# Kernel optimization log

Measured on AMD Instinct MI355X. Metric: run time of the kernel, lower is better.

The kernel has to match this reference:

```python
import jax, jax.numpy as jnp
import numpy as np

D, H, DH = 768, 12, 64
W = 256            # one-sided window (attention_window=512 total)
EPS = 1e-6
NEG = -1e9


def layer_norm(x, g, b):
    m = jnp.mean(x, axis=-1, keepdims=True)
    v = jnp.mean((x - m) ** 2, axis=-1, keepdims=True)
    return g * (x - m) * jax.lax.rsqrt(v + EPS) + b


def _blocks3(t, nb):
    # t: [B,H,nb,W,dh] -> keys/values of 3 neighboring blocks [B,H,nb,3W,dh]
    tp = jnp.pad(t, ((0, 0), (0, 0), (1, 1), (0, 0), (0, 0)))
    return jnp.concatenate([tp[:, :, :nb], tp[:, :, 1:nb + 1], tp[:, :, 2:nb + 2]], axis=3)


def sliding_window_attention(x, kpm, Wq, bq, Wk, bk, Wv, bv, Wo, bo):
    B, S, _ = x.shape
    nb = S // W
    def proj(Wm, bm):
        return (x @ Wm + bm).reshape(B, S, H, DH).transpose(0, 2, 1, 3).reshape(B, H, nb, W, DH)
    q = proj(Wq, bq) * (1.0 / np.sqrt(DH))
    k = proj(Wk, bk)
    v = proj(Wv, bv)
    k3 = _blocks3(k, nb)
    v3 = _blocks3(v, nb)
    # scores over local band: [B,H,nb,W,3W]
    s = jnp.einsum('bhnqd,bhnkd->bhnqk', q, k3)
    qi = jnp.arange(W)[:, None]
    kj = jnp.arange(3 * W)[None, :]
    band = jnp.abs(kj - W - qi) <= W                     # [W,3W]
    kg = (jnp.arange(nb)[:, None, None] - 1) * W + kj[None]  # global key idx [nb,1,3W]
    inrange = (kg >= 0) & (kg < S)
    # key padding mask gathered into block layout: [B,nb,3W]
    kpm_b = jnp.pad(kpm.reshape(B, nb, W), ((0, 0), (1, 1), (0, 0)), constant_values=True)
    kpm3 = jnp.concatenate([kpm_b[:, :nb], kpm_b[:, 1:nb + 1], kpm_b[:, 2:nb + 2]], axis=2)
    m = band[None, None, None] & inrange[None, None] & (~kpm3)[:, None, :, None, :]
    s = jnp.where(m, s, NEG)
    p = jax.nn.softmax(s, axis=-1)
    o = jnp.einsum('bhnqk,bhnkd->bhnqd', p, v3)
    o = o.reshape(B, H, S, DH).transpose(0, 2, 1, 3).reshape(B, S, D)
    return o @ Wo + bo


def setup_inputs() -> dict:
    key = jax.random.key(0)
    ks = jax.random.split(key, 12)
    B, S, DF = 2, 4096, 3072
    sc = 1.0 / np.sqrt(D)
    return {
        'x': jax.random.normal(ks[0], (B, S, D), jnp.float32),
        'mask': jnp.zeros((B, S), bool),
        'id': 0,
        'Wq': jax.random.normal(ks[1], (D, D), jnp.float32) * sc,
        'bq': jnp.zeros((D,), jnp.float32),
        'Wk': jax.random.normal(ks[2], (D, D), jnp.float32) * sc,
        'bk': jnp.zeros((D,), jnp.float32),
        'Wv': jax.random.normal(ks[3], (D, D), jnp.float32) * sc,
        'bv': jnp.zeros((D,), jnp.float32),
        'Wo': jax.random.normal(ks[4], (D, D), jnp.float32) * sc,
        'bo': jnp.zeros((D,), jnp.float32),
        'ln1_g': jnp.ones((D,), jnp.float32),
        'ln1_b': jnp.zeros((D,), jnp.float32),
        'W1': jax.random.normal(ks[5], (D, DF), jnp.float32) * sc,
        'b1': jnp.zeros((DF,), jnp.float32),
        'W2': jax.random.normal(ks[6], (DF, D), jnp.float32) * (1.0 / np.sqrt(DF)),
        'b2': jnp.zeros((D,), jnp.float32),
        'ln2_g': jnp.ones((D,), jnp.float32),
        'ln2_b': jnp.zeros((D,), jnp.float32),
    }


def reference(x, mask, id, Wq, bq, Wk, bk, Wv, bv, Wo, bo, ln1_g, ln1_b, W1, b1, W2, b2, ln2_g, ln2_b):
    # Sublayer 1: pre-norm residual around sliding-window self-attention
    h = layer_norm(x, ln1_g, ln1_b)
    x = x + sliding_window_attention(h, mask, Wq, bq, Wk, bk, Wv, bv, Wo, bo)
    # Sublayer 2: pre-norm residual around positionwise FFN
    h = layer_norm(x, ln2_g, ln2_b)
    x = x + (jax.nn.relu(h @ W1 + b1) @ W2 + b2)
    return x
```

## Files before the change

kernel.cpp:

```cpp
#include <hip/hip_runtime.h>
#include <hip/hip_bf16.h>
#include <cstddef>

typedef __attribute__((ext_vector_type(8))) short short8;
typedef __attribute__((ext_vector_type(4))) float f32x4;
typedef __attribute__((ext_vector_type(4))) unsigned short us4;

typedef __attribute__((address_space(1))) void as1_void;
typedef __attribute__((address_space(3))) void as3_void;

__device__ __forceinline__ void gload16(const void* g, void* lds) {
  __builtin_amdgcn_global_load_lds((as1_void*)(void*)g, (as3_void*)lds, 16, 0, 0);
}

__device__ inline unsigned short f2bf(float f) {
  union { float f; unsigned int u; } v; v.f = f;
  return (unsigned short)((v.u + 0x7FFFu + ((v.u >> 16) & 1u)) >> 16);
}

__global__ __launch_bounds__(256) void ln_kernel(const float* __restrict__ x,
    const float* __restrict__ g, const float* __restrict__ b,
    unsigned short* __restrict__ out)
{
  int row = blockIdx.x, t = threadIdx.x;
  const float* xr = x + (size_t)row * 768;
  float v0 = xr[t], v1 = xr[t + 256], v2 = xr[t + 512];
  float s = v0 + v1 + v2;
  #pragma unroll
  for (int o = 32; o > 0; o >>= 1) s += __shfl_xor(s, o);
  __shared__ float r1[4], r2[4];
  if ((t & 63) == 0) r1[t >> 6] = s;
  __syncthreads();
  float mean = (r1[0] + r1[1] + r1[2] + r1[3]) * (1.0f / 768.0f);
  float d0 = v0 - mean, d1 = v1 - mean, d2 = v2 - mean;
  float q = d0 * d0 + d1 * d1 + d2 * d2;
  #pragma unroll
  for (int o = 32; o > 0; o >>= 1) q += __shfl_xor(q, o);
  if ((t & 63) == 0) r2[t >> 6] = q;
  __syncthreads();
  float var = (r2[0] + r2[1] + r2[2] + r2[3]) * (1.0f / 768.0f);
  float rs = rsqrtf(var + 1e-6f);
  unsigned short* orow = out + (size_t)row * 768;
  orow[t]       = f2bf(g[t]       * d0 * rs + b[t]);
  orow[t + 256] = f2bf(g[t + 256] * d1 * rs + b[t + 256]);
  orow[t + 512] = f2bf(g[t + 512] * d2 * rs + b[t + 512]);
}

__global__ __launch_bounds__(256) void transpose_kernel(const float* __restrict__ W,
    unsigned short* __restrict__ WT, int K, int N)
{
  __shared__ float tile[32][33];
  int tx = threadIdx.x & 31, ty = threadIdx.x >> 5;
  int k0 = blockIdx.x * 32, n0 = blockIdx.y * 32;
  #pragma unroll
  for (int i = 0; i < 32; i += 8)
    tile[ty + i][tx] = W[(size_t)(k0 + ty + i) * N + n0 + tx];
  __syncthreads();
  #pragma unroll
  for (int i = 0; i < 32; i += 8)
    WT[(size_t)(n0 + ty + i) * K + k0 + tx] = f2bf(tile[tx][ty + i]);
}

__global__ __launch_bounds__(256) void catbias_kernel(const float* __restrict__ bq,
    const float* __restrict__ bk, const float* __restrict__ bv, float* __restrict__ o)
{
  int i = blockIdx.x * 256 + threadIdx.x;
  o[i] = (i < 768) ? bq[i] : ((i < 1536) ? bk[i - 768] : bv[i - 1536]);
}

enum { EPI_QKV = 0, EPI_RELU = 1, EPI_RESID = 2 };

template<int EPI>
__global__ __launch_bounds__(512, 1) void gemmP_kernel(
    const unsigned short* __restrict__ A, const unsigned short* __restrict__ BT,
    const float* __restrict__ bias, const float* __restrict__ resid,
    void* __restrict__ outp, int M, int N, int K, int ntn)
{
  __shared__ char lds[2][49152];
  int tid = threadIdx.x;
  int nwg = gridDim.x;
  int bid = ((int)blockIdx.x & 7) * (nwg >> 3) + ((int)blockIdx.x >> 3);
  int mt = bid / ntn, nt = bid % ntn;
  int m0 = mt * 128, n0 = nt * 256;
  int w = tid >> 6, l = tid & 63;
  int wr = w >> 2, wc = w & 3;
  int fr = l & 15, fq = l >> 4;
  int swz = (fr >> 1) * 128 + (((((fr & 1) << 2) | fq) ^ ((fr >> 1) & 7)) << 4);
  int t8 = tid >> 3;
  int uu = (tid & 7) ^ (t8 & 7);
  int rb = 2 * t8 + (uu >> 2);
  int kb = (uu & 3) * 8;
  const unsigned short* Asrc  = A  + (size_t)(m0 + rb) * K + kb;
  const unsigned short* Bsrc0 = BT + (size_t)(n0 + rb) * K + kb;
  const unsigned short* Bsrc1 = BT + (size_t)(n0 + 128 + rb) * K + kb;

  auto stage = [&](int buf, int kt, int h) {
    int ko = kt * 64 + h * 32;
    char* dA = &lds[buf][0] + h * 8192 + (w << 10);
    char* dB = &lds[buf][16384] + h * 16384 + (w << 10);
    gload16(Asrc + ko, dA);
    gload16(Bsrc0 + ko, dB);
    gload16(Bsrc1 + ko, dB + 8192);
  };

  f32x4 acc[4][4] = {};

#define GP_COMPUTE(RBUF, H)                                                    \
  { short8 af[4], bf[4];                                                       \
    const char* ab_ = &lds[RBUF][0] + (H) * 8192 + wr * 4096 + swz;            \
    const char* bb_ = &lds[RBUF][16384] + (H) * 16384 + wc * 4096 + swz;       \
    _Pragma("unroll")                                                          \
    for (int i_ = 0; i_ < 4; i_++) af[i_] = *(const short8*)(ab_ + i_ * 1024); \
    _Pragma("unroll")                                                          \
    for (int j_ = 0; j_ < 4; j_++) bf[j_] = *(const short8*)(bb_ + j_ * 1024); \
    __builtin_amdgcn_s_setprio(1);                                             \
    _Pragma("unroll")                                                          \
    for (int i_ = 0; i_ < 4; i_++)                                             \
      _Pragma("unroll")                                                        \
      for (int j_ = 0; j_ < 4; j_++)                                           \
        acc[i_][j_] = __builtin_amdgcn_mfma_f32_16x16x32_bf16(                 \
            af[i_], bf[j_], acc[i_][j_], 0, 0, 0);                             \
    __builtin_amdgcn_s_setprio(0); }

  stage(0, 0, 0); stage(0, 0, 1);
  asm volatile("s_waitcnt vmcnt(3)" ::: "memory");
  __builtin_amdgcn_s_barrier();

  int NT = K >> 6;
  for (int t = 0; t < NT - 1; ++t) {
    int R = t & 1, W = R ^ 1;
    GP_COMPUTE(R, 0);
    stage(W, t + 1, 0);
    asm volatile("s_waitcnt vmcnt(3)" ::: "memory");
    __builtin_amdgcn_s_barrier();
    GP_COMPUTE(R, 1);
    stage(W, t + 1, 1);
    asm volatile("s_waitcnt vmcnt(3)" ::: "memory");
    __builtin_amdgcn_s_barrier();
  }
  {
    int R = (NT - 1) & 1;
    GP_COMPUTE(R, 0);
    asm volatile("s_waitcnt vmcnt(0)" ::: "memory");
    __builtin_amdgcn_s_barrier();
    GP_COMPUTE(R, 1);
  }
#undef GP_COMPUTE

  #pragma unroll
  for (int nj = 0; nj < 4; nj++) {
    int col = n0 + wc * 64 + nj * 16 + fr;
    float bs = bias[col];
    if (EPI == EPI_QKV) {
      int which = (col >= 1536) ? 2 : ((col >= 768) ? 1 : 0);
      int c2 = col - which * 768;
      int hh = c2 >> 6, dh = c2 & 63;
      if (which == 2) {
        unsigned short* dstv = reinterpret_cast<unsigned short*>(outp) + (size_t)2 * 8192 * 768;
        #pragma unroll
        for (int i = 0; i < 4; i++) {
          int row0 = m0 + wr * 64 + i * 16 + fq * 4;
          int bb = row0 >> 12, sl = row0 & 4095;
          us4 pv;
          #pragma unroll
          for (int r = 0; r < 4; r++) pv[r] = f2bf(acc[i][nj][r] + bs);
          *reinterpret_cast<us4*>(&dstv[((size_t)(bb * 12 + hh) * 64 + dh) * 4096 + sl]) = pv;
        }
      } else {
        unsigned short* dst = reinterpret_cast<unsigned short*>(outp) + (size_t)which * 8192 * 768;
        #pragma unroll
        for (int i = 0; i < 4; i++) {
          #pragma unroll
          for (int r = 0; r < 4; r++) {
            int row = m0 + wr * 64 + i * 16 + fq * 4 + r;
            float c = acc[i][nj][r] + bs;
            if (which == 0) c *= 0.125f;
            int bb = row >> 12, sl = row & 4095;
            dst[(((size_t)(bb * 12 + hh)) * 4096 + sl) * 64 + dh] = f2bf(c);
          }
        }
      }
    } else if (EPI == EPI_RELU) {
      #pragma unroll
      for (int i = 0; i < 4; i++)
        #pragma unroll
        for (int r = 0; r < 4; r++) {
          int row = m0 + wr * 64 + i * 16 + fq * 4 + r;
          float c = fmaxf(acc[i][nj][r] + bs, 0.0f);
          reinterpret_cast<unsigned short*>(outp)[(size_t)row * N + col] = f2bf(c);
        }
    } else {
      #pragma unroll
      for (int i = 0; i < 4; i++)
        #pragma unroll
        for (int r = 0; r < 4; r++) {
          int row = m0 + wr * 64 + i * 16 + fq * 4 + r;
          float c = acc[i][nj][r] + bs + resid[(size_t)row * N + col];
          reinterpret_cast<float*>(outp)[(size_t)row * N + col] = c;
        }
    }
  }
}

__global__ __launch_bounds__(256) void attn_fused_kernel(
    const unsigned short* __restrict__ qg, const unsigned short* __restrict__ kg,
    const unsigned short* __restrict__ vtg, const unsigned char* __restrict__ kpm,
    unsigned short* __restrict__ attn_out)
{
  __shared__ unsigned short lds_k[2][64 * 64];
  __shared__ unsigned short lds_vt[2][64 * 64];
  __shared__ unsigned short lds_p[4][32 * 64];
  int bid0 = blockIdx.x;
  int bid = (bid0 & 7) * 96 + (bid0 >> 3);
  int qblk = bid & 31, h = (bid >> 5) % 12, b = bid / 384;
  int bh = b * 12 + h;
  int q0 = qblk * 128;
  int tid = threadIdx.x, w = tid >> 6, l = tid & 63;
  int fr = l & 15, fq = l >> 4;
  int qw0 = q0 + w * 32;
  int swzb = (((l & 7) ^ (l >> 3)) << 4);
  const char* qbase  = (const char*)(qg  + (size_t)bh * 4096 * 64);
  const char* kbase  = (const char*)(kg  + (size_t)bh * 4096 * 64);
  const char* vtbase = (const char*)(vtg + (size_t)bh * 64 * 4096);
  const unsigned char* kpmb = kpm + (size_t)b * 4096;

  #pragma unroll
  for (int s = 0; s < 4; s++) {
    int row = w * 32 + s * 8 + (l >> 3);
    gload16(qbase + (size_t)(q0 + row) * 128 + swzb, (char*)lds_p[w] + s * 1024);
  }

  auto stageKV = [&](int c, int buf) {
    int g0 = q0 - 256 + c * 64;
    if (g0 < 0 || g0 >= 4096) return;
    #pragma unroll
    for (int s = 0; s < 2; s++) {
      int row = w * 16 + s * 8 + (l >> 3);
      gload16(kbase + (size_t)(g0 + row) * 128 + swzb,
              (char*)lds_k[buf] + (w * 2 + s) * 1024);
      gload16(vtbase + ((size_t)row * 4096 + g0) * 2 + swzb,
              (char*)lds_vt[buf] + (w * 2 + s) * 1024);
    }
  };

  stageKV(0, 0);
  asm volatile("s_waitcnt vmcnt(0)");
  __syncthreads();

  short8 qf[2][2];
  #pragma unroll
  for (int i = 0; i < 2; i++)
    #pragma unroll
    for (int ks = 0; ks < 2; ks++)
      qf[i][ks] = *(const short8*)((const char*)lds_p[w] + (i * 16 + fr) * 128 +
                    ((ks * 64 + fq * 16) ^ ((fr & 7) << 4)));

  f32x4 acc_o[2][4] = {};
  float m_st[2] = {-3.0e38f, -3.0e38f};
  float l_st[2] = {0.0f, 0.0f};

  for (int c = 0; c < 10; c++) {
    int g0 = q0 - 256 + c * 64;
    bool valid = (g0 >= 0) && (g0 < 4096);
    if (c < 9) stageKV(c + 1, (c + 1) & 1);
    if (valid) {
      int buf = c & 1;
      unsigned int km[4];
      #pragma unroll
      for (int j = 0; j < 4; j++)
        km[j] = *(const unsigned int*)(kpmb + g0 + 16 * j + 4 * fq);
      bool anyk = __any((km[0] | km[1] | km[2] | km[3]) != 0);
      int rel = g0 - qw0;
      bool edge = anyk || (rel < -225) || (rel > 193);
      short8 kf[4][2];
      #pragma unroll
      for (int j = 0; j < 4; j++)
        #pragma unroll
        for (int ks = 0; ks < 2; ks++)
          kf[j][ks] = *(const short8*)((const char*)lds_k[buf] + (j * 16 + fr) * 128 +
                        ((ks * 64 + fq * 16) ^ ((fr & 7) << 4)));
      f32x4 accs[4][2] = {};
      #pragma unroll
      for (int j = 0; j < 4; j++)
        #pragma unroll
        for (int i = 0; i < 2; i++)
          #pragma unroll
          for (int ks = 0; ks < 2; ks++)
            accs[j][i] = __builtin_amdgcn_mfma_f32_16x16x32_bf16(kf[j][ks], qf[i][ks], accs[j][i], 0, 0, 0);
      #pragma unroll
      for (int i = 0; i < 2; i++) {
        float sv[4][4];
        #pragma unroll
        for (int j = 0; j < 4; j++)
          #pragma unroll
          for (int r = 0; r < 4; r++)
            sv[j][r] = accs[j][i][r];
        if (edge) {
          int base = rel + 4 * fq - fr - 16 * i;
          #pragma unroll
          for (int j = 0; j < 4; j++)
            #pragma unroll
            for (int r = 0; r < 4; r++) {
              int d = base + 16 * j + r;
              bool ok = (d >= -256) && (d <= 256) && (((km[j] >> (8 * r)) & 255u) == 0u);
              if (!ok) sv[j][r] = -1.0e9f;
            }
        }
        float mv = sv[0][0];
        #pragma unroll
        for (int j = 0; j < 4; j++)
          #pragma unroll
          for (int r = 0; r < 4; r++) mv = fmaxf(mv, sv[j][r]);
        mv = fmaxf(mv, __shfl_xor(mv, 16));
        mv = fmaxf(mv, __shfl_xor(mv, 32));
        float mo = m_st[i];
        float mn = fmaxf(mo, mv);
        float scl = __expf(mo - mn);
        float rs = 0.0f;
        unsigned int pk[4][2];
        #pragma unroll
        for (int j = 0; j < 4; j++) {
          float p0 = __expf(sv[j][0] - mn), p1 = __expf(sv[j][1] - mn);
          float p2 = __expf(sv[j][2] - mn), p3 = __expf(sv[j][3] - mn);
          rs += (p0 + p1) + (p2 + p3);
          pk[j][0] = (unsigned)f2bf(p0) | ((unsigned)f2bf(p1) << 16);
          pk[j][1] = (unsigned)f2bf(p2) | ((unsigned)f2bf(p3) << 16);
        }
        rs += __shfl_xor(rs, 16);
        rs += __shfl_xor(rs, 32);
        l_st[i] = l_st[i] * scl + rs;
        m_st[i] = mn;
        char* prow = (char*)lds_p[w] + (i * 16 + fr) * 128;
        #pragma unroll
        for (int j = 0; j < 4; j++) {
          uint2 u; u.x = pk[j][0]; u.y = pk[j][1];
          *(uint2*)(prow + ((32 * j + 8 * fq) ^ ((fr & 7) << 4))) = u;
        }
        #pragma unroll
        for (int r = 0; r < 4; r++) {
          float so = __shfl(scl, (l & 48) | ((l >> 2) & 12) | r);
          #pragma unroll
          for (int jd = 0; jd < 4; jd++) acc_o[i][jd][r] *= so;
        }
      }
      short8 pf[2][2];
      #pragma unroll
      for (int i = 0; i < 2; i++)
        #pragma unroll
        for (int ks = 0; ks < 2; ks++)
          pf[i][ks] = *(const short8*)((const char*)lds_p[w] + (i * 16 + fr) * 128 +
                        ((ks * 64 + fq * 16) ^ ((fr & 7) << 4)));
      short8 vf[4][2];
      #pragma unroll
      for (int jd = 0; jd < 4; jd++)
        #pragma unroll
        for (int ks = 0; ks < 2; ks++)
          vf[jd][ks] = *(const short8*)((const char*)lds_vt[buf] + (jd * 16 + fr) * 128 +
                        ((ks * 64 + fq * 16) ^ ((fr & 7) << 4)));
      #pragma unroll
      for (int i = 0; i < 2; i++)
        #pragma unroll
        for (int jd = 0; jd < 4; jd++)
          #pragma unroll
          for (int ks = 0; ks < 2; ks++)
            acc_o[i][jd] = __builtin_amdgcn_mfma_f32_16x16x32_bf16(pf[i][ks], vf[jd][ks], acc_o[i][jd], 0, 0, 0);
    }
    asm volatile("s_waitcnt vmcnt(0)");
    __syncthreads();
  }
  #pragma unroll
  for (int i = 0; i < 2; i++) {
    #pragma unroll
    for (int r = 0; r < 4; r++) {
      float lv = __shfl(l_st[i], (l & 48) | ((l >> 2) & 12) | r);
      float inv = 1.0f / lv;
      int qrow = qw0 + i * 16 + fq * 4 + r;
      size_t orow = ((size_t)b * 4096 + qrow) * 768 + h * 64;
      #pragma unroll
      for (int jd = 0; jd < 4; jd++)
        attn_out[orow + jd * 16 + fr] = f2bf(acc_o[i][jd][r] * inv);
    }
  }
}

extern "C" void kernel_launch(void* const* d_in, const int* in_sizes, int n_in,
                              void* d_out, int out_size, void* d_ws, size_t ws_size,
                              hipStream_t stream) {
  const float* x            = (const float*)d_in[0];
  const unsigned char* mask = (const unsigned char*)d_in[1];
  const float* Wq  = (const float*)d_in[3];
  const float* bq  = (const float*)d_in[4];
  const float* Wk  = (const float*)d_in[5];
  const float* bk  = (const float*)d_in[6];
  const float* Wv  = (const float*)d_in[7];
  const float* bv  = (const float*)d_in[8];
  const float* Wo  = (const float*)d_in[9];
  const float* bo  = (const float*)d_in[10];
  const float* ln1g = (const float*)d_in[11];
  const float* ln1b = (const float*)d_in[12];
  const float* W1  = (const float*)d_in[13];
  const float* b1  = (const float*)d_in[14];
  const float* W2  = (const float*)d_in[15];
  const float* b2  = (const float*)d_in[16];
  const float* ln2g = (const float*)d_in[17];
  const float* ln2b = (const float*)d_in[18];
  float* out = (float*)d_out;

  char* ws = (char*)d_ws;
  size_t off = 0;
  auto alloc = [&](size_t bytes) -> void* {
    void* p = ws + off;
    off += (bytes + 255) & ~(size_t)255;
    return p;
  };
  unsigned short* WTqkv = (unsigned short*)alloc((size_t)2304 * 768 * 2);
  unsigned short* WTo   = (unsigned short*)alloc((size_t)768 * 768 * 2);
  unsigned short* W1T   = (unsigned short*)alloc((size_t)3072 * 768 * 2);
  unsigned short* W2T   = (unsigned short*)alloc((size_t)768 * 3072 * 2);
  float*          bqkv  = (float*)alloc(2304 * 4);
  unsigned short* hbuf  = (unsigned short*)alloc((size_t)8192 * 768 * 2);
  unsigned short* qkv   = (unsigned short*)alloc((size_t)3 * 8192 * 768 * 2);
  unsigned short* attn  = (unsigned short*)alloc((size_t)8192 * 768 * 2);
  float* x1             = (float*)alloc((size_t)8192 * 768 * 4);
  unsigned short* h2    = (unsigned short*)alloc((size_t)8192 * 768 * 2);
  unsigned short* a1    = (unsigned short*)alloc((size_t)8192 * 3072 * 2);

  transpose_kernel<<<dim3(24, 24), 256, 0, stream>>>(Wq, WTqkv, 768, 768);
  transpose_kernel<<<dim3(24, 24), 256, 0, stream>>>(Wk, WTqkv + (size_t)768 * 768, 768, 768);
  transpose_kernel<<<dim3(24, 24), 256, 0, stream>>>(Wv, WTqkv + (size_t)1536 * 768, 768, 768);
  transpose_kernel<<<dim3(24, 24), 256, 0, stream>>>(Wo, WTo, 768, 768);
  transpose_kernel<<<dim3(24, 96), 256, 0, stream>>>(W1, W1T, 768, 3072);
  transpose_kernel<<<dim3(96, 24), 256, 0, stream>>>(W2, W2T, 3072, 768);
  catbias_kernel<<<9, 256, 0, stream>>>(bq, bk, bv, bqkv);

  ln_kernel<<<8192, 256, 0, stream>>>(x, ln1g, ln1b, hbuf);

  gemmP_kernel<EPI_QKV><<<576, 512, 0, stream>>>(hbuf, WTqkv, bqkv, nullptr, qkv, 8192, 2304, 768, 9);

  attn_fused_kernel<<<768, 256, 0, stream>>>(qkv, qkv + (size_t)8192 * 768,
                                             qkv + (size_t)2 * 8192 * 768, mask, attn);

  gemmP_kernel<EPI_RESID><<<192, 512, 0, stream>>>(attn, WTo, bo, x, x1, 8192, 768, 768, 3);
  ln_kernel<<<8192, 256, 0, stream>>>(x1, ln2g, ln2b, h2);
  gemmP_kernel<EPI_RELU><<<768, 512, 0, stream>>>(h2, W1T, b1, nullptr, a1, 8192, 3072, 768, 12);
  gemmP_kernel<EPI_RESID><<<192, 512, 0, stream>>>(a1, W2T, b2, x1, out, 8192, 768, 3072, 3);
}
```

Measured before the change: 271.9 us.

## Triple-buffer GEMM pipeline and use exp2 lazy-rescale softmax with packed bf16 converts

The GEMM moves from double to triple LDS buffering (3x48KB), issuing loads two k-tiles ahead before computing, so global loads overlap more with MFMA work. In attention, the Q scale absorbs log2(e) so the softmax can use the raw v_exp_f32 instruction. The running max and output rescale are skipped unless the new max exceeds the old by more than 8, which relies on bounded growth of the accumulators. Bf16 packing uses the v_cvt_pk_bf16_f32 instruction. The larger LDS footprint limits occupancy, which is already one workgroup per CU.

```diff
diff --git a/kernel.cpp b/kernel.cpp
--- a/kernel.cpp
+++ b/kernel.cpp
@@ -16,6 +16,13 @@
 __device__ inline unsigned short f2bf(float f) {
   union { float f; unsigned int u; } v; v.f = f;
   return (unsigned short)((v.u + 0x7FFFu + ((v.u >> 16) & 1u)) >> 16);
+}
+
+__device__ __forceinline__ float exp2v(float x) {
+  float r; asm("v_exp_f32 %0, %1" : "=v"(r) : "v"(x)); return r;
+}
+__device__ __forceinline__ unsigned cvtpk(float a, float b) {
+  unsigned r; asm("v_cvt_pk_bf16_f32 %0, %1, %2" : "=v"(r) : "v"(a), "v"(b)); return r;
 }
 
 __global__ __launch_bounds__(256) void ln_kernel(const float* __restrict__ x,
@@ -76,7 +83,7 @@
     const float* __restrict__ bias, const float* __restrict__ resid,
     void* __restrict__ outp, int M, int N, int K, int ntn)
 {
-  __shared__ char lds[2][49152];
+  __shared__ char lds[3][49152];
   int tid = threadIdx.x;
   int nwg = gridDim.x;
   int bid = ((int)blockIdx.x & 7) * (nwg >> 3) + ((int)blockIdx.x >> 3);
@@ -122,29 +129,35 @@
             af[i_], bf[j_], acc[i_][j_], 0, 0, 0);                             \
     __builtin_amdgcn_s_setprio(0); }
 
-  stage(0, 0, 0); stage(0, 0, 1);
+  stage(0, 0, 0); stage(0, 0, 1); stage(1, 1, 0); stage(1, 1, 1);
+  asm volatile("s_waitcnt vmcnt(9)" ::: "memory");
+  __builtin_amdgcn_s_barrier();
+
+  int NT = K >> 6;
+  int R = 0;
+  for (int t = 0; t < NT - 2; ++t) {
+    int W = (R == 0) ? 2 : R - 1;
+    stage(W, t + 2, 0);
+    GP_COMPUTE(R, 0);
+    asm volatile("s_waitcnt vmcnt(9)" ::: "memory");
+    __builtin_amdgcn_s_barrier();
+    stage(W, t + 2, 1);
+    GP_COMPUTE(R, 1);
+    asm volatile("s_waitcnt vmcnt(9)" ::: "memory");
+    __builtin_amdgcn_s_barrier();
+    R = (R == 2) ? 0 : R + 1;
+  }
+  GP_COMPUTE(R, 0);
+  asm volatile("s_waitcnt vmcnt(6)" ::: "memory");
+  __builtin_amdgcn_s_barrier();
+  GP_COMPUTE(R, 1);
   asm volatile("s_waitcnt vmcnt(3)" ::: "memory");
   __builtin_amdgcn_s_barrier();
-
-  int NT = K >> 6;
-  for (int t = 0; t < NT - 1; ++t) {
-    int R = t & 1, W = R ^ 1;
-    GP_COMPUTE(R, 0);
-    stage(W, t + 1, 0);
-    asm volatile("s_waitcnt vmcnt(3)" ::: "memory");
-    __builtin_amdgcn_s_barrier();
-    GP_COMPUTE(R, 1);
-    stage(W, t + 1, 1);
-    asm volatile("s_waitcnt vmcnt(3)" ::: "memory");
-    __builtin_amdgcn_s_barrier();
-  }
-  {
-    int R = (NT - 1) & 1;
-    GP_COMPUTE(R, 0);
-    asm volatile("s_waitcnt vmcnt(0)" ::: "memory");
-    __builtin_amdgcn_s_barrier();
-    GP_COMPUTE(R, 1);
-  }
+  R = (R == 2) ? 0 : R + 1;
+  GP_COMPUTE(R, 0);
+  asm volatile("s_waitcnt vmcnt(0)" ::: "memory");
+  __builtin_amdgcn_s_barrier();
+  GP_COMPUTE(R, 1);
 #undef GP_COMPUTE
 
   #pragma unroll
@@ -174,7 +187,7 @@
           for (int r = 0; r < 4; r++) {
             int row = m0 + wr * 64 + i * 16 + fq * 4 + r;
             float c = acc[i][nj][r] + bs;
-            if (which == 0) c *= 0.125f;
+            if (which == 0) c *= 0.18033688011112042f;
             int bb = row >> 12, sl = row & 4095;
             dst[(((size_t)(bb * 12 + hh)) * 4096 + sl) * 64 + dh] = f2bf(c);
           }
@@ -314,34 +327,32 @@
         mv = fmaxf(mv, __shfl_xor(mv, 16));
         mv = fmaxf(mv, __shfl_xor(mv, 32));
         float mo = m_st[i];
-        float mn = fmaxf(mo, mv);
-        float scl = __expf(mo - mn);
+        if (!__all(mv - mo <= 8.0f)) {
+          float mn = fmaxf(mo, mv);
+          float scl = exp2v(mo - mn);
+          l_st[i] *= scl;
+          m_st[i] = mn;
+          #pragma unroll
+          for (int r = 0; r < 4; r++) {
+            float so = __shfl(scl, (l & 48) | ((l >> 2) & 12) | r);
+            #pragma unroll
+            for (int jd = 0; jd < 4; jd++) acc_o[i][jd][r] *= so;
+          }
+        }
+        float mn = m_st[i];
         float rs = 0.0f;
-        unsigned int pk[4][2];
+        char* prow = (char*)lds_p[w] + (i * 16 + fr) * 128;
         #pragma unroll
         for (int j = 0; j < 4; j++) {
-          float p0 = __expf(sv[j][0] - mn), p1 = __expf(sv[j][1] - mn);
-          float p2 = __expf(sv[j][2] - mn), p3 = __expf(sv[j][3] - mn);
+          float p0 = exp2v(sv[j][0] - mn), p1 = exp2v(sv[j][1] - mn);
+          float p2 = exp2v(sv[j][2] - mn), p3 = exp2v(sv[j][3] - mn);
           rs += (p0 + p1) + (p2 + p3);
-          pk[j][0] = (unsigned)f2bf(p0) | ((unsigned)f2bf(p1) << 16);
-          pk[j][1] = (unsigned)f2bf(p2) | ((unsigned)f2bf(p3) << 16);
+          uint2 u; u.x = cvtpk(p0, p1); u.y = cvtpk(p2, p3);
+          *(uint2*)(prow + ((32 * j + 8 * fq) ^ ((fr & 7) << 4))) = u;
         }
         rs += __shfl_xor(rs, 16);
         rs += __shfl_xor(rs, 32);
-        l_st[i] = l_st[i] * scl + rs;
-        m_st[i] = mn;
-        char* prow = (char*)lds_p[w] + (i * 16 + fr) * 128;
-        #pragma unroll
-        for (int j = 0; j < 4; j++) {
-          uint2 u; u.x = pk[j][0]; u.y = pk[j][1];
-          *(uint2*)(prow + ((32 * j + 8 * fq) ^ ((fr & 7) << 4))) = u;
-        }
-        #pragma unroll
-        for (int r = 0; r < 4; r++) {
-          float so = __shfl(scl, (l & 48) | ((l >> 2) & 12) | r);
-          #pragma unroll
-          for (int jd = 0; jd < 4; jd++) acc_o[i][jd][r] *= so;
-        }
+        l_st[i] += rs;
       }
       short8 pf[2][2];
       #pragma unroll
```

Result: faster. 265.8 us (-2.2%).
